# Kernel optimization log

Hardware: AMD Instinct MI355X
Metric: run time of the kernel (lower is better)

Reference implementation:

```python
import jax, jax.numpy as jnp
import numpy as np

B, OBS, LAT, NXT, E, HG, H = 8192, 128, 32, 128, 8, 256, 256


def setup_inputs() -> dict:
    key = jax.random.key(0)
    ks = jax.random.split(key, 20)
    d_in = OBS + LAT

    def w(k, shape, fan_in):
        return jax.random.uniform(k, shape, jnp.float32, -1.0, 1.0) * (np.sqrt(3.0) / np.sqrt(fan_in)).astype(np.float32)

    inp = {
        "x": jax.random.normal(ks[0], (B, OBS), jnp.float32),
        "z": jax.random.normal(ks[1], (B, LAT), jnp.float32),
        # gating MLP: (obs+lat) -> hg -> hg -> hg -> E
        "gw0": w(ks[2], (d_in, HG), d_in), "gb0": jnp.zeros((HG,), jnp.float32),
        "gw1": w(ks[3], (HG, HG), HG),    "gb1": jnp.zeros((HG,), jnp.float32),
        "gw2": w(ks[4], (HG, HG), HG),    "gb2": jnp.zeros((HG,), jnp.float32),
        "gw3": w(ks[5], (HG, E), HG),     "gb3": jnp.zeros((E,), jnp.float32),
        # expert weight stacks (kaiming-uniform-style init, bias = 0.01)
        "w0": w(ks[6], (E, d_in, H), d_in * H),      "b0": jnp.full((E, H), 0.01, jnp.float32),
        "w1": w(ks[7], (E, H + LAT, H), (H + LAT) * H), "b1": jnp.full((E, H), 0.01, jnp.float32),
        "w2": w(ks[8], (E, H + LAT, NXT), (H + LAT) * NXT), "b2": jnp.full((E, NXT), 0.01, jnp.float32),
    }
    return inp


def reference(x, z, gw0, gb0, gw1, gb1, gw2, gb2, gw3, gb3, w0, b0, w1, b1, w2, b2):
    xz = jnp.concatenate((x, z), axis=1)  # [B, obs+lat]
    # gating MLP (ELU activations, linear head) -> softmax coefficients over experts
    g = jax.nn.elu(xz @ gw0 + gb0)
    g = jax.nn.elu(g @ gw1 + gb1)
    g = jax.nn.elu(g @ gw2 + gb2)
    coef = jax.nn.softmax(g @ gw3 + gb3, axis=1)  # [B, E]

    layer_out = x
    for w, b, act in ((w0, b0, jax.nn.elu), (w1, b1, jax.nn.elu), (w2, b2, None)):
        inp = jnp.concatenate((layer_out, z), axis=1)  # [B, i]
        # coefficient-weighted expert mixing fused with the per-sample matvec:
        # equals (coef @ flat_weight).view(B,i,o) consumed by baddbmm in the original
        out = jnp.einsum('bi,eio,be->bo', inp, w, coef) + coef @ b
        layer_out = act(out) if act is not None else out
    return layer_out
```

## Files before the change

kernel.cpp:

```cpp
#include <hip/hip_runtime.h>
#include <hip/hip_bf16.h>

typedef _Float16 half_t;
typedef __attribute__((ext_vector_type(8))) _Float16 half8;
typedef __attribute__((ext_vector_type(4))) _Float16 half4;
typedef __attribute__((ext_vector_type(4))) float float4v;
typedef __attribute__((ext_vector_type(4))) unsigned int uint4v;

#define BSZ 8192

template <int EXP, int MODE>
__global__ __launch_bounds__(256, 4) void moe_gemm2(
    const half_t* __restrict__ A, int lda, const half_t* __restrict__ W, int Npad,
    const float* __restrict__ bias, int biasN, const float* __restrict__ coef,
    int K, int Nvalid, half_t* __restrict__ Oh, float* __restrict__ Of, int ldo) {
    __shared__ __align__(16) half_t sB[EXP * 64 * 8];
    __shared__ float sCf[EXP == 8 ? 128 * 8 : 8];

    const int tid  = threadIdx.x;
    const int row0 = blockIdx.x * 128;
    const int col0 = blockIdx.y * 16;
    const int lane = tid & 63, wv = tid >> 6;
    const int l15  = lane & 15, quad = lane >> 4;

    const bool sact = (EXP == 8) || (tid < 32);
    const int se = (EXP == 8) ? (tid >> 5) : 0;
    const int sn = (tid >> 1) & 15;
    const int sp = (tid & 1) * 2;
    const half_t* wsrc = &W[((size_t)se * Npad + col0 + sn) * K + sp * 8];
    half_t* wdst = &sB[(se * 64 + sn * 4 + sp) * 8];

    if (EXP == 8)
        *(uint4v*)&sCf[tid * 4] = *(const uint4v*)&coef[(size_t)row0 * 8 + tid * 4];

    float4v acc[EXP][2];
#pragma unroll
    for (int e = 0; e < EXP; ++e)
#pragma unroll
        for (int mt = 0; mt < 2; ++mt) acc[e][mt] = (float4v){0.f, 0.f, 0.f, 0.f};

    for (int kc = 0; kc < K; kc += 32) {
        half8 a[2];
#pragma unroll
        for (int mt = 0; mt < 2; ++mt)
            a[mt] = *(const half8*)&A[(size_t)(row0 + wv * 32 + mt * 16 + l15) * lda +
                                      kc + quad * 8];
        __syncthreads();
        if (sact) {
            *(uint4v*)wdst       = *(const uint4v*)&wsrc[kc];
            *(uint4v*)&wdst[8]   = *(const uint4v*)&wsrc[kc + 8];
        }
        __syncthreads();
#pragma unroll
        for (int e = 0; e < EXP; ++e) {
            half8 b = *(const half8*)&sB[(e * 64 + l15 * 4 + quad) * 8];
#pragma unroll
            for (int mt = 0; mt < 2; ++mt)
                acc[e][mt] = __builtin_amdgcn_mfma_f32_16x16x32_f16(a[mt], b, acc[e][mt], 0, 0, 0);
        }
    }

    const int col = col0 + l15;
    const bool cok = col < Nvalid;
    float bv[EXP];
#pragma unroll
    for (int e = 0; e < EXP; ++e) bv[e] = cok ? bias[e * biasN + col] : 0.f;

#pragma unroll
    for (int mt = 0; mt < 2; ++mt) {
#pragma unroll
        for (int r = 0; r < 4; ++r) {
            const int rl = wv * 32 + mt * 16 + quad * 4 + r;
            float val;
            if (EXP == 1) {
                val = acc[0][mt][r] + bv[0];
            } else {
                const float4v c0 = *(const float4v*)&sCf[rl * 8];
                const float4v c1 = *(const float4v*)&sCf[rl * 8 + 4];
                val = 0.f;
#pragma unroll
                for (int e = 0; e < 4; ++e) val += c0[e] * (acc[e][mt][r] + bv[e]);
#pragma unroll
                for (int e = 4; e < 8; ++e) val += c1[e - 4] * (acc[e][mt][r] + bv[e]);
            }
            if (cok) {
                const size_t o = (size_t)(row0 + rl) * ldo + col;
                if (MODE == 0) {
                    val = (val > 0.f) ? val : expm1f(val);
                    Oh[o] = (half_t)val;
                } else {
                    Of[o] = val;
                }
            }
        }
    }
}

__global__ __launch_bounds__(256) void conv_inputs(
    const float* __restrict__ x, const float* __restrict__ z,
    half_t* __restrict__ A0, half_t* __restrict__ P, half_t* __restrict__ Q) {
    int idx = blockIdx.x * 256 + threadIdx.x;
    int b = idx / 192, c = idx % 192;
    float v = (c < 128) ? x[(size_t)b * 128 + c] : z[(size_t)b * 32 + ((c - 128) & 31)];
    half_t h = (half_t)v;
    if (c < 160) {
        A0[(size_t)b * 160 + c] = h;
    } else {
        size_t o = (size_t)b * 288 + 96 + c;
        P[o] = h;
        Q[o] = h;
    }
}

struct WDesc { const float* src; half_t* dst; int K, N, Npad, blk0; };
struct WPack { WDesc d[7]; };

__global__ __launch_bounds__(256) void conv_w_all(WPack pk) {
    __shared__ float t[32][33];
    const int bid = blockIdx.x;
    int di = 0;
#pragma unroll
    for (int i = 1; i < 7; ++i)
        if (bid >= pk.d[i].blk0) di = i;
    const WDesc d = pk.d[di];
    const int ntiles = d.Npad / 32, ktiles = d.K / 32;
    int local = bid - d.blk0;
    const int e  = local / (ktiles * ntiles);
    local %= ktiles * ntiles;
    const int k0 = (local / ntiles) * 32, n0 = (local % ntiles) * 32;
    const int tr = threadIdx.x >> 3;
    const int tc = (threadIdx.x & 7) * 4;

    float4 v = {0.f, 0.f, 0.f, 0.f};
    if (n0 + tc < d.N)
        v = *(const float4*)&d.src[((size_t)e * d.K + k0 + tr) * d.N + n0 + tc];
    t[tr][tc] = v.x; t[tr][tc + 1] = v.y; t[tr][tc + 2] = v.z; t[tr][tc + 3] = v.w;
    __syncthreads();
    half4 h;
#pragma unroll
    for (int i = 0; i < 4; ++i) h[i] = (half_t)t[tc + i][tr];
    *(half4*)&d.dst[((size_t)e * d.Npad + n0 + tr) * d.K + k0 + tc] = h;
}

__global__ __launch_bounds__(256) void softmax8_kernel(const float* __restrict__ logits,
                                                       float* __restrict__ coef) {
    int b = blockIdx.x * 256 + threadIdx.x;
    if (b >= BSZ) return;
    float v[8], m = -1e30f;
#pragma unroll
    for (int e = 0; e < 8; ++e) { v[e] = logits[b * 8 + e]; m = fmaxf(m, v[e]); }
    float s = 0.f;
#pragma unroll
    for (int e = 0; e < 8; ++e) { v[e] = expf(v[e] - m); s += v[e]; }
    float inv = 1.f / s;
#pragma unroll
    for (int e = 0; e < 8; ++e) coef[b * 8 + e] = v[e] * inv;
}

extern "C" void kernel_launch(void* const* d_in, const int* in_sizes, int n_in,
                              void* d_out, int out_size, void* d_ws, size_t ws_size,
                              hipStream_t stream) {
    const float* x   = (const float*)d_in[0];
    const float* z   = (const float*)d_in[1];
    const float* gw0 = (const float*)d_in[2];
    const float* gb0 = (const float*)d_in[3];
    const float* gw1 = (const float*)d_in[4];
    const float* gb1 = (const float*)d_in[5];
    const float* gw2 = (const float*)d_in[6];
    const float* gb2 = (const float*)d_in[7];
    const float* gw3 = (const float*)d_in[8];
    const float* gb3 = (const float*)d_in[9];
    const float* w0  = (const float*)d_in[10];
    const float* b0  = (const float*)d_in[11];
    const float* w1  = (const float*)d_in[12];
    const float* b1  = (const float*)d_in[13];
    const float* w2  = (const float*)d_in[14];
    const float* b2  = (const float*)d_in[15];

    char* p = (char*)d_ws;
    auto take = [&](size_t bytes) { char* r = p; p += bytes; return r; };
    half_t* A0  = (half_t*)take((size_t)BSZ * 160 * 2);
    half_t* P   = (half_t*)take((size_t)BSZ * 288 * 2);
    half_t* Q   = (half_t*)take((size_t)BSZ * 288 * 2);
    half_t* Wg0 = (half_t*)take((size_t)256 * 160 * 2);
    half_t* Wg1 = (half_t*)take((size_t)256 * 256 * 2);
    half_t* Wg2 = (half_t*)take((size_t)256 * 256 * 2);
    half_t* Wg3 = (half_t*)take((size_t)32 * 256 * 2);
    half_t* W0  = (half_t*)take((size_t)8 * 256 * 160 * 2);
    half_t* W1  = (half_t*)take((size_t)8 * 256 * 288 * 2);
    half_t* W2  = (half_t*)take((size_t)8 * 128 * 288 * 2);
    float* logits = (float*)take((size_t)BSZ * 8 * 4);
    float* coef   = (float*)take((size_t)BSZ * 8 * 4);
    float* out    = (float*)d_out;

    WPack pk;
    int blk = 0;
    auto mk = [&](int i, const float* s, half_t* dst, int K, int N, int Npad, int E) {
        pk.d[i] = WDesc{s, dst, K, N, Npad, blk};
        blk += E * (K / 32) * (Npad / 32);
    };
    mk(0, gw0, Wg0, 160, 256, 256, 1);
    mk(1, gw1, Wg1, 256, 256, 256, 1);
    mk(2, gw2, Wg2, 256, 256, 256, 1);
    mk(3, gw3, Wg3, 256, 8, 32, 1);
    mk(4, w0, W0, 160, 256, 256, 8);
    mk(5, w1, W1, 288, 256, 256, 8);
    mk(6, w2, W2, 288, 128, 128, 8);

    dim3 b256(256);
    conv_inputs<<<dim3(BSZ * 192 / 256), b256, 0, stream>>>(x, z, A0, P, Q);
    conv_w_all<<<dim3(blk), b256, 0, stream>>>(pk);

    moe_gemm2<1, 0><<<dim3(64, 16), b256, 0, stream>>>(A0, 160, Wg0, 256, gb0, 256,
                                                       nullptr, 160, 256, P, nullptr, 288);
    moe_gemm2<1, 0><<<dim3(64, 16), b256, 0, stream>>>(P, 288, Wg1, 256, gb1, 256,
                                                       nullptr, 256, 256, Q, nullptr, 288);
    moe_gemm2<1, 0><<<dim3(64, 16), b256, 0, stream>>>(Q, 288, Wg2, 256, gb2, 256,
                                                       nullptr, 256, 256, P, nullptr, 288);
    moe_gemm2<1, 1><<<dim3(64, 1), b256, 0, stream>>>(P, 288, Wg3, 32, gb3, 8,
                                                      nullptr, 256, 8, nullptr, logits, 8);
    softmax8_kernel<<<dim3(BSZ / 256), b256, 0, stream>>>(logits, coef);
    moe_gemm2<8, 0><<<dim3(64, 16), b256, 0, stream>>>(A0, 160, W0, 256, b0, 256,
                                                       coef, 160, 256, Q, nullptr, 288);
    moe_gemm2<8, 0><<<dim3(64, 16), b256, 0, stream>>>(Q, 288, W1, 256, b1, 256,
                                                       coef, 288, 256, P, nullptr, 288);
    moe_gemm2<8, 1><<<dim3(64, 8), b256, 0, stream>>>(P, 288, W2, 128, b2, 128,
                                                      coef, 288, 128, nullptr, out, 128);
}
```

Before: 159.8 us.

## Fuse whole gating and expert MLP chain into one per-row-block kernel

Replaces the chain of separate GEMM, input-conversion and softmax kernels with a single kernel. Each 32-row block keeps its activations in shared memory across all seven layers and reads weights straight from global/L2 with register double-buffering. This removes the intermediate activation round-trips through global memory and most kernel launch gaps. In exchange only 256 blocks are launched, each wave re-reads every weight from L2 with no LDS sharing, and the 8-expert layers hold large accumulator and B-register sets that may lower occupancy.

```diff
diff --git a/kernel.cpp b/kernel.cpp
--- a/kernel.cpp
+++ b/kernel.cpp
@@ -5,111 +5,151 @@
 typedef __attribute__((ext_vector_type(8))) _Float16 half8;
 typedef __attribute__((ext_vector_type(4))) _Float16 half4;
 typedef __attribute__((ext_vector_type(4))) float float4v;
-typedef __attribute__((ext_vector_type(4))) unsigned int uint4v;
 
 #define BSZ 8192
 
-template <int EXP, int MODE>
-__global__ __launch_bounds__(256, 4) void moe_gemm2(
-    const half_t* __restrict__ A, int lda, const half_t* __restrict__ W, int Npad,
-    const float* __restrict__ bias, int biasN, const float* __restrict__ coef,
-    int K, int Nvalid, half_t* __restrict__ Oh, float* __restrict__ Of, int ldo) {
-    __shared__ __align__(16) half_t sB[EXP * 64 * 8];
-    __shared__ float sCf[EXP == 8 ? 128 * 8 : 8];
-
-    const int tid  = threadIdx.x;
-    const int row0 = blockIdx.x * 128;
-    const int col0 = blockIdx.y * 16;
+template <int EXP, int CH, int NSTR, int ACT, int DST>
+__device__ __forceinline__ void layer_fused(
+    const half_t* sSrc, int sstr, const half_t* __restrict__ W, int Npad,
+    const float* __restrict__ bias, int biasN, int nvalid, const float* sCf,
+    half_t* sDst, int dstr, float* sLogF, float* __restrict__ gOut, int ldg,
+    int row0, int wv, int l15, int quad) {
+    constexpr int K = CH * 32;
+    for (int s = wv; s < NSTR; s += 4) {
+        const int col = s * 16 + l15;
+        const bool cok = col < nvalid;
+        float bv[EXP];
+#pragma unroll
+        for (int e = 0; e < EXP; ++e) bv[e] = cok ? bias[e * biasN + col] : 0.f;
+
+        float4v acc[EXP][2];
+#pragma unroll
+        for (int e = 0; e < EXP; ++e)
+#pragma unroll
+            for (int mt = 0; mt < 2; ++mt) acc[e][mt] = (float4v){0.f, 0.f, 0.f, 0.f};
+
+        const half_t* wb = &W[(size_t)(s * 16 + l15) * K + quad * 8];
+        half8 a0 = *(const half8*)&sSrc[l15 * sstr + quad * 8];
+        half8 a1 = *(const half8*)&sSrc[(16 + l15) * sstr + quad * 8];
+        half8 b[EXP];
+#pragma unroll
+        for (int e = 0; e < EXP; ++e) b[e] = *(const half8*)&wb[(size_t)e * Npad * K];
+
+#pragma unroll
+        for (int c = 0; c < CH; ++c) {
+            half8 a0n, a1n, bn[EXP];
+            if (c + 1 < CH) {
+                const int kc = (c + 1) * 32;
+                a0n = *(const half8*)&sSrc[l15 * sstr + kc + quad * 8];
+                a1n = *(const half8*)&sSrc[(16 + l15) * sstr + kc + quad * 8];
+#pragma unroll
+                for (int e = 0; e < EXP; ++e)
+                    bn[e] = *(const half8*)&wb[(size_t)e * Npad * K + kc];
+            }
+#pragma unroll
+            for (int e = 0; e < EXP; ++e) {
+                acc[e][0] = __builtin_amdgcn_mfma_f32_16x16x32_f16(a0, b[e], acc[e][0], 0, 0, 0);
+                acc[e][1] = __builtin_amdgcn_mfma_f32_16x16x32_f16(a1, b[e], acc[e][1], 0, 0, 0);
+            }
+            if (c + 1 < CH) {
+                a0 = a0n; a1 = a1n;
+#pragma unroll
+                for (int e = 0; e < EXP; ++e) b[e] = bn[e];
+            }
+        }
+#pragma unroll
+        for (int mt = 0; mt < 2; ++mt)
+#pragma unroll
+            for (int r = 0; r < 4; ++r) {
+                const int rl = mt * 16 + quad * 4 + r;
+                float val;
+                if (EXP == 1) {
+                    val = acc[0][mt][r] + bv[0];
+                } else {
+                    val = 0.f;
+#pragma unroll
+                    for (int e = 0; e < EXP; ++e)
+                        val += sCf[rl * 8 + e] * (acc[e][mt][r] + bv[e]);
+                }
+                if (DST == 0) {
+                    if (ACT) val = (val > 0.f) ? val : expm1f(val);
+                    sDst[rl * dstr + col] = (half_t)val;
+                } else if (DST == 1) {
+                    if (cok) sLogF[rl * 8 + col] = val;
+                } else {
+                    if (cok) gOut[(size_t)(row0 + rl) * ldg + col] = val;
+                }
+            }
+    }
+}
+
+__global__ __launch_bounds__(256) void fused_mann(
+    const float* __restrict__ x, const float* __restrict__ z,
+    const half_t* __restrict__ Wg0, const half_t* __restrict__ Wg1,
+    const half_t* __restrict__ Wg2, const half_t* __restrict__ Wg3,
+    const float* __restrict__ gb0, const float* __restrict__ gb1,
+    const float* __restrict__ gb2, const float* __restrict__ gb3,
+    const half_t* __restrict__ W0, const half_t* __restrict__ W1,
+    const half_t* __restrict__ W2, const float* __restrict__ b0,
+    const float* __restrict__ b1, const float* __restrict__ b2,
+    float* __restrict__ out) {
+    __shared__ __align__(16) half_t sA0[32 * 168];
+    __shared__ __align__(16) half_t sBuf0[32 * 296];
+    __shared__ __align__(16) half_t sBuf1[32 * 296];
+    __shared__ float sLog[32 * 8];
+    __shared__ float sCf[32 * 8];
+
+    const int tid = threadIdx.x;
+    const int row0 = blockIdx.x * 32;
     const int lane = tid & 63, wv = tid >> 6;
-    const int l15  = lane & 15, quad = lane >> 4;
-
-    const bool sact = (EXP == 8) || (tid < 32);
-    const int se = (EXP == 8) ? (tid >> 5) : 0;
-    const int sn = (tid >> 1) & 15;
-    const int sp = (tid & 1) * 2;
-    const half_t* wsrc = &W[((size_t)se * Npad + col0 + sn) * K + sp * 8];
-    half_t* wdst = &sB[(se * 64 + sn * 4 + sp) * 8];
-
-    if (EXP == 8)
-        *(uint4v*)&sCf[tid * 4] = *(const uint4v*)&coef[(size_t)row0 * 8 + tid * 4];
-
-    float4v acc[EXP][2];
-#pragma unroll
-    for (int e = 0; e < EXP; ++e)
-#pragma unroll
-        for (int mt = 0; mt < 2; ++mt) acc[e][mt] = (float4v){0.f, 0.f, 0.f, 0.f};
-
-    for (int kc = 0; kc < K; kc += 32) {
-        half8 a[2];
-#pragma unroll
-        for (int mt = 0; mt < 2; ++mt)
-            a[mt] = *(const half8*)&A[(size_t)(row0 + wv * 32 + mt * 16 + l15) * lda +
-                                      kc + quad * 8];
-        __syncthreads();
-        if (sact) {
-            *(uint4v*)wdst       = *(const uint4v*)&wsrc[kc];
-            *(uint4v*)&wdst[8]   = *(const uint4v*)&wsrc[kc + 8];
-        }
-        __syncthreads();
-#pragma unroll
-        for (int e = 0; e < EXP; ++e) {
-            half8 b = *(const half8*)&sB[(e * 64 + l15 * 4 + quad) * 8];
-#pragma unroll
-            for (int mt = 0; mt < 2; ++mt)
-                acc[e][mt] = __builtin_amdgcn_mfma_f32_16x16x32_f16(a[mt], b, acc[e][mt], 0, 0, 0);
-        }
-    }
-
-    const int col = col0 + l15;
-    const bool cok = col < Nvalid;
-    float bv[EXP];
-#pragma unroll
-    for (int e = 0; e < EXP; ++e) bv[e] = cok ? bias[e * biasN + col] : 0.f;
-
-#pragma unroll
-    for (int mt = 0; mt < 2; ++mt) {
-#pragma unroll
-        for (int r = 0; r < 4; ++r) {
-            const int rl = wv * 32 + mt * 16 + quad * 4 + r;
-            float val;
-            if (EXP == 1) {
-                val = acc[0][mt][r] + bv[0];
-            } else {
-                const float4v c0 = *(const float4v*)&sCf[rl * 8];
-                const float4v c1 = *(const float4v*)&sCf[rl * 8 + 4];
-                val = 0.f;
-#pragma unroll
-                for (int e = 0; e < 4; ++e) val += c0[e] * (acc[e][mt][r] + bv[e]);
-#pragma unroll
-                for (int e = 4; e < 8; ++e) val += c1[e - 4] * (acc[e][mt][r] + bv[e]);
-            }
-            if (cok) {
-                const size_t o = (size_t)(row0 + rl) * ldo + col;
-                if (MODE == 0) {
-                    val = (val > 0.f) ? val : expm1f(val);
-                    Oh[o] = (half_t)val;
-                } else {
-                    Of[o] = val;
-                }
-            }
-        }
-    }
-}
-
-__global__ __launch_bounds__(256) void conv_inputs(
-    const float* __restrict__ x, const float* __restrict__ z,
-    half_t* __restrict__ A0, half_t* __restrict__ P, half_t* __restrict__ Q) {
-    int idx = blockIdx.x * 256 + threadIdx.x;
-    int b = idx / 192, c = idx % 192;
-    float v = (c < 128) ? x[(size_t)b * 128 + c] : z[(size_t)b * 32 + ((c - 128) & 31)];
-    half_t h = (half_t)v;
-    if (c < 160) {
-        A0[(size_t)b * 160 + c] = h;
-    } else {
-        size_t o = (size_t)b * 288 + 96 + c;
-        P[o] = h;
-        Q[o] = h;
-    }
+    const int l15 = lane & 15, quad = lane >> 4;
+
+    for (int i = tid; i < 32 * 160; i += 256) {
+        int r = i / 160, c = i % 160;
+        float v = (c < 128) ? x[(size_t)(row0 + r) * 128 + c]
+                            : z[(size_t)(row0 + r) * 32 + (c - 128)];
+        sA0[r * 168 + c] = (half_t)v;
+    }
+    for (int i = tid; i < 32 * 32; i += 256) {
+        int r = i >> 5, c = i & 31;
+        half_t h = (half_t)z[(size_t)(row0 + r) * 32 + c];
+        sBuf0[r * 296 + 256 + c] = h;
+        sBuf1[r * 296 + 256 + c] = h;
+    }
+    __syncthreads();
+
+    layer_fused<1, 5, 16, 1, 0>(sA0, 168, Wg0, 256, gb0, 256, 256, nullptr,
+                                sBuf0, 296, nullptr, nullptr, 0, row0, wv, l15, quad);
+    __syncthreads();
+    layer_fused<1, 8, 16, 1, 0>(sBuf0, 296, Wg1, 256, gb1, 256, 256, nullptr,
+                                sBuf1, 296, nullptr, nullptr, 0, row0, wv, l15, quad);
+    __syncthreads();
+    layer_fused<1, 8, 16, 1, 0>(sBuf1, 296, Wg2, 256, gb2, 256, 256, nullptr,
+                                sBuf0, 296, nullptr, nullptr, 0, row0, wv, l15, quad);
+    __syncthreads();
+    layer_fused<1, 8, 1, 0, 1>(sBuf0, 296, Wg3, 32, gb3, 8, 8, nullptr,
+                               nullptr, 0, sLog, nullptr, 0, row0, wv, l15, quad);
+    __syncthreads();
+    if (tid < 32) {
+        float v[8], m = -1e30f;
+#pragma unroll
+        for (int e = 0; e < 8; ++e) { v[e] = sLog[tid * 8 + e]; m = fmaxf(m, v[e]); }
+        float sum = 0.f;
+#pragma unroll
+        for (int e = 0; e < 8; ++e) { v[e] = expf(v[e] - m); sum += v[e]; }
+        float inv = 1.f / sum;
+#pragma unroll
+        for (int e = 0; e < 8; ++e) sCf[tid * 8 + e] = v[e] * inv;
+    }
+    __syncthreads();
+    layer_fused<8, 5, 16, 1, 0>(sA0, 168, W0, 256, b0, 256, 256, sCf,
+                                sBuf1, 296, nullptr, nullptr, 0, row0, wv, l15, quad);
+    __syncthreads();
+    layer_fused<8, 9, 16, 1, 0>(sBuf1, 296, W1, 256, b1, 256, 256, sCf,
+                                sBuf0, 296, nullptr, nullptr, 0, row0, wv, l15, quad);
+    __syncthreads();
+    layer_fused<8, 9, 8, 0, 2>(sBuf0, 296, W2, 128, b2, 128, 128, sCf,
+                               nullptr, 0, nullptr, out, 128, row0, wv, l15, quad);
 }
 
 struct WDesc { const float* src; half_t* dst; int K, N, Npad, blk0; };
@@ -125,7 +165,7 @@
     const WDesc d = pk.d[di];
     const int ntiles = d.Npad / 32, ktiles = d.K / 32;
     int local = bid - d.blk0;
-    const int e  = local / (ktiles * ntiles);
+    const int e = local / (ktiles * ntiles);
     local %= ktiles * ntiles;
     const int k0 = (local / ntiles) * 32, n0 = (local % ntiles) * 32;
     const int tr = threadIdx.x >> 3;
@@ -140,21 +180,6 @@
 #pragma unroll
     for (int i = 0; i < 4; ++i) h[i] = (half_t)t[tc + i][tr];
     *(half4*)&d.dst[((size_t)e * d.Npad + n0 + tr) * d.K + k0 + tc] = h;
-}
-
-__global__ __launch_bounds__(256) void softmax8_kernel(const float* __restrict__ logits,
-                                                       float* __restrict__ coef) {
-    int b = blockIdx.x * 256 + threadIdx.x;
-    if (b >= BSZ) return;
-    float v[8], m = -1e30f;
-#pragma unroll
-    for (int e = 0; e < 8; ++e) { v[e] = logits[b * 8 + e]; m = fmaxf(m, v[e]); }
-    float s = 0.f;
-#pragma unroll
-    for (int e = 0; e < 8; ++e) { v[e] = expf(v[e] - m); s += v[e]; }
-    float inv = 1.f / s;
-#pragma unroll
-    for (int e = 0; e < 8; ++e) coef[b * 8 + e] = v[e] * inv;
 }
 
 extern "C" void kernel_launch(void* const* d_in, const int* in_sizes, int n_in,
@@ -179,9 +204,6 @@
 
     char* p = (char*)d_ws;
     auto take = [&](size_t bytes) { char* r = p; p += bytes; return r; };
-    half_t* A0  = (half_t*)take((size_t)BSZ * 160 * 2);
-    half_t* P   = (half_t*)take((size_t)BSZ * 288 * 2);
-    half_t* Q   = (half_t*)take((size_t)BSZ * 288 * 2);
     half_t* Wg0 = (half_t*)take((size_t)256 * 160 * 2);
     half_t* Wg1 = (half_t*)take((size_t)256 * 256 * 2);
     half_t* Wg2 = (half_t*)take((size_t)256 * 256 * 2);
@@ -189,9 +211,7 @@
     half_t* W0  = (half_t*)take((size_t)8 * 256 * 160 * 2);
     half_t* W1  = (half_t*)take((size_t)8 * 256 * 288 * 2);
     half_t* W2  = (half_t*)take((size_t)8 * 128 * 288 * 2);
-    float* logits = (float*)take((size_t)BSZ * 8 * 4);
-    float* coef   = (float*)take((size_t)BSZ * 8 * 4);
-    float* out    = (float*)d_out;
+    float* out  = (float*)d_out;
 
     WPack pk;
     int blk = 0;
@@ -208,22 +228,8 @@
     mk(6, w2, W2, 288, 128, 128, 8);
 
     dim3 b256(256);
-    conv_inputs<<<dim3(BSZ * 192 / 256), b256, 0, stream>>>(x, z, A0, P, Q);
     conv_w_all<<<dim3(blk), b256, 0, stream>>>(pk);
-
-    moe_gemm2<1, 0><<<dim3(64, 16), b256, 0, stream>>>(A0, 160, Wg0, 256, gb0, 256,
-                                                       nullptr, 160, 256, P, nullptr, 288);
-    moe_gemm2<1, 0><<<dim3(64, 16), b256, 0, stream>>>(P, 288, Wg1, 256, gb1, 256,
-                                                       nullptr, 256, 256, Q, nullptr, 288);
-    moe_gemm2<1, 0><<<dim3(64, 16), b256, 0, stream>>>(Q, 288, Wg2, 256, gb2, 256,
-                                                       nullptr, 256, 256, P, nullptr, 288);
-    moe_gemm2<1, 1><<<dim3(64, 1), b256, 0, stream>>>(P, 288, Wg3, 32, gb3, 8,
-                                                      nullptr, 256, 8, nullptr, logits, 8);
-    softmax8_kernel<<<dim3(BSZ / 256), b256, 0, stream>>>(logits, coef);
-    moe_gemm2<8, 0><<<dim3(64, 16), b256, 0, stream>>>(A0, 160, W0, 256, b0, 256,
-                                                       coef, 160, 256, Q, nullptr, 288);
-    moe_gemm2<8, 0><<<dim3(64, 16), b256, 0, stream>>>(Q, 288, W1, 256, b1, 256,
-                                                       coef, 288, 256, P, nullptr, 288);
-    moe_gemm2<8, 1><<<dim3(64, 8), b256, 0, stream>>>(P, 288, W2, 128, b2, 128,
-                                                      coef, 288, 128, nullptr, out, 128);
-}
+    fused_mann<<<dim3(BSZ / 32), b256, 0, stream>>>(
+        x, z, Wg0, Wg1, Wg2, Wg3, gb0, gb1, gb2, gb3,
+        W0, W1, W2, b0, b1, b2, out);
+}
```

Result: slower. 211.8 us (+32.5%).
